# Performance work log

Hardware: AMD Instinct MI355X
Metric: run time of the kernel (lower is better)

## Reference

```python
import jax, jax.numpy as jnp
import numpy as np

D = 1024
N_HEAD = 16
EXP = 4
EPS = 1e-6


def setup_inputs() -> dict:
    key = jax.random.key(0)
    ks = jax.random.split(key, 7)
    s = 0.02
    return {
        "x": jax.random.normal(ks[0], (2, 2048, D), dtype=jnp.float32),
        "w_qkv": jax.random.normal(ks[1], (3 * D, D), dtype=jnp.float32) * s,
        "w_o": jax.random.normal(ks[2], (D, D), dtype=jnp.float32) * s,
        "w_up": jax.random.normal(ks[3], (EXP * D, D), dtype=jnp.float32) * s,
        "w_gate": jax.random.normal(ks[4], (EXP * D, D), dtype=jnp.float32) * s,
        "w_down": jax.random.normal(ks[5], (D, EXP * D), dtype=jnp.float32) * s,
        "scale1": jnp.ones((D,), dtype=jnp.float32),
        "scale2": jnp.ones((D,), dtype=jnp.float32),
    }


def rmsnorm(x, scale):
    return x / jnp.sqrt(jnp.mean(x * x, axis=-1, keepdims=True) + EPS) * scale


def attention(x, w_qkv, w_o):
    b, s, d = x.shape
    dh = d // N_HEAD
    qkv = x @ w_qkv.T  # [b,s,3d]
    q, k, v = jnp.split(qkv, 3, axis=-1)
    # [b,h,s,dh]
    q = q.reshape(b, s, N_HEAD, dh).transpose(0, 2, 1, 3)
    k = k.reshape(b, s, N_HEAD, dh).transpose(0, 2, 1, 3)
    v = v.reshape(b, s, N_HEAD, dh).transpose(0, 2, 1, 3)
    scores = jnp.einsum("bhqd,bhkd->bhqk", q, k) / jnp.sqrt(jnp.float32(dh))
    causal = jnp.tril(jnp.ones((s, s), dtype=bool))
    scores = jnp.where(causal, scores, -jnp.inf)
    attn = jax.nn.softmax(scores, axis=-1)
    out = jnp.einsum("bhqk,bhkd->bhqd", attn, v)
    out = out.transpose(0, 2, 1, 3).reshape(b, s, d)
    return out @ w_o.T


def mlp(x, w_up, w_gate, w_down):
    return (x @ w_up.T * jax.nn.silu(x @ w_gate.T)) @ w_down.T


def reference(x, w_qkv, w_o, w_up, w_gate, w_down, scale1, scale2):
    x = x + attention(rmsnorm(x, scale1), w_qkv, w_o)
    return x + mlp(rmsnorm(x, scale2), w_up, w_gate, w_down)
```

## Files before the change

kernel.cpp:

```cpp
#include <hip/hip_runtime.h>


typedef __attribute__((ext_vector_type(8))) short short8;
typedef __attribute__((ext_vector_type(4))) float floatx4;

#define EPI_NONE 0
#define EPI_RES  1
#define EPI_GATE 2
#define EPI_QKV  3

#define QSCALE 0.1803368801f

__device__ __forceinline__ float b2f(unsigned short u) {
  union { unsigned int i; float f; } c; c.i = ((unsigned int)u) << 16; return c.f;
}
__device__ __forceinline__ unsigned short f2b(float f) {
  union { float f; unsigned int u; } c; c.f = f;
  unsigned int r = 0x7fffu + ((c.u >> 16) & 1u);
  return (unsigned short)((c.u + r) >> 16);
}
__device__ __forceinline__ unsigned int f2b2(float a, float b) {
  return (unsigned int)f2b(a) | ((unsigned int)f2b(b) << 16);
}

__device__ __forceinline__ void load_lds16(const void* g, void* l) {
  __builtin_amdgcn_global_load_lds(
      (const __attribute__((address_space(1))) unsigned int*)g,
      (__attribute__((address_space(3))) unsigned int*)l, 16, 0, 0);
}

__global__ __launch_bounds__(256)
void cvt_all_kernel(const float* __restrict__ wq, const float* __restrict__ wo,
                    const float* __restrict__ wu, const float* __restrict__ wg,
                    const float* __restrict__ wd,
                    unsigned short* __restrict__ oq, unsigned short* __restrict__ oo,
                    unsigned short* __restrict__ ou, unsigned short* __restrict__ og,
                    unsigned short* __restrict__ od) {
  int i = blockIdx.x * 256 + threadIdx.x;
  const float* src; unsigned short* dst; int k;
  if (i < 786432)        { src = wq; dst = oq; k = i; }
  else if (i < 1048576)  { src = wo; dst = oo; k = i - 786432; }
  else if (i < 2097152)  { src = wu; dst = ou; k = i - 1048576; }
  else if (i < 3145728)  { src = wg; dst = og; k = i - 2097152; }
  else                   { src = wd; dst = od; k = i - 3145728; }
  float4 v = ((const float4*)src)[k];
  ushort4 o;
  o.x = f2b(v.x); o.y = f2b(v.y); o.z = f2b(v.z); o.w = f2b(v.w);
  ((ushort4*)dst)[k] = o;
}

__global__ __launch_bounds__(256)
void rmsnorm_kernel(const float* __restrict__ x,
                    const float* __restrict__ scale,
                    unsigned short* __restrict__ y) {
  const int row = blockIdx.x;
  const int tid = threadIdx.x;
  const int base = row * 1024 + tid * 4;
  float4 v = *(const float4*)(x + base);
  float ss = v.x*v.x + v.y*v.y + v.z*v.z + v.w*v.w;
#pragma unroll
  for (int d = 32; d > 0; d >>= 1) ss += __shfl_down(ss, d);
  __shared__ float red[4];
  const int wave = tid >> 6, lane = tid & 63;
  if (lane == 0) red[wave] = ss;
  __syncthreads();
  float tot = red[0] + red[1] + red[2] + red[3];
  float rs = rsqrtf(tot * (1.0f/1024.0f) + 1e-6f);
  float4 sv = *(const float4*)(scale + tid * 4);
  ushort4 o;
  o.x = f2b(v.x * rs * sv.x);
  o.y = f2b(v.y * rs * sv.y);
  o.z = f2b(v.z * rs * sv.z);
  o.w = f2b(v.w * rs * sv.w);
  *(ushort4*)(y + base) = o;
}

__global__ __launch_bounds__(256)
void rmsnorm_res2_kernel(const float* __restrict__ x,
                         const float* __restrict__ p0,
                         const float* __restrict__ p1,
                         const float* __restrict__ scale,
                         float* __restrict__ x1,
                         unsigned short* __restrict__ y) {
  const int row = blockIdx.x;
  const int tid = threadIdx.x;
  const int base = row * 1024 + tid * 4;
  float4 a = *(const float4*)(x + base);
  float4 b = *(const float4*)(p0 + base);
  float4 c = *(const float4*)(p1 + base);
  float4 v;
  v.x = a.x + b.x + c.x; v.y = a.y + b.y + c.y;
  v.z = a.z + b.z + c.z; v.w = a.w + b.w + c.w;
  *(float4*)(x1 + base) = v;
  float ss = v.x*v.x + v.y*v.y + v.z*v.z + v.w*v.w;
#pragma unroll
  for (int d = 32; d > 0; d >>= 1) ss += __shfl_down(ss, d);
  __shared__ float red[4];
  const int wave = tid >> 6, lane = tid & 63;
  if (lane == 0) red[wave] = ss;
  __syncthreads();
  float tot = red[0] + red[1] + red[2] + red[3];
  float rs = rsqrtf(tot * (1.0f/1024.0f) + 1e-6f);
  float4 sv = *(const float4*)(scale + tid * 4);
  ushort4 o;
  o.x = f2b(v.x * rs * sv.x);
  o.y = f2b(v.y * rs * sv.y);
  o.z = f2b(v.z * rs * sv.z);
  o.w = f2b(v.w * rs * sv.w);
  *(ushort4*)(y + base) = o;
}

__global__ __launch_bounds__(256)
void reduce_out_kernel(const float* __restrict__ x1,
                       const float* __restrict__ p1,
                       float* outp) {
  int i = blockIdx.x * 256 + threadIdx.x;
  float4 a = ((const float4*)x1)[i];
  float4 b = ((const float4*)p1)[i];
  float4 c = ((float4*)outp)[i];
  float4 v;
  v.x = a.x + b.x + c.x; v.y = a.y + b.y + c.y;
  v.z = a.z + b.z + c.z; v.w = a.w + b.w + c.w;
  ((float4*)outp)[i] = v;
}

template<int EPI, typename OutT, typename ResT>
__global__ __launch_bounds__(256)
void gemm_bt(const unsigned short* __restrict__ A,
             const unsigned short* __restrict__ B,
             OutT* C, const ResT* R, unsigned short* VT,
             int M, int N, int K, int ldc) {
  __shared__ __align__(16) unsigned short As[128 * 32];
  __shared__ __align__(16) unsigned short Bs[128 * 32];
  const int tid = threadIdx.x;
  const int wave = tid >> 6;
  const int lane = tid & 63;
  const int m0 = blockIdx.y * 128;
  const int n0 = blockIdx.x * 128;
  const int wm = (wave & 1) * 64;
  const int wn = (wave >> 1) * 64;
  const int frow = lane & 15;
  const int fk = (lane >> 4) * 8;

  floatx4 acc[4][4];
#pragma unroll
  for (int i = 0; i < 4; ++i)
#pragma unroll
    for (int j = 0; j < 4; ++j) acc[i][j] = (floatx4){0.f, 0.f, 0.f, 0.f};

  const int srow = lane >> 2;
  const int scol = (lane & 3) * 8;
  const unsigned short* Ag  = A + (size_t)(m0 + wave * 16 + srow) * K + scol;
  const unsigned short* Ag2 = A + (size_t)(m0 + (wave + 4) * 16 + srow) * K + scol;
  const unsigned short* Bg  = B + (size_t)(n0 + wave * 16 + srow) * K + scol;
  const unsigned short* Bg2 = B + (size_t)(n0 + (wave + 4) * 16 + srow) * K + scol;

  for (int k0 = 0; k0 < K; k0 += 32) {
    __syncthreads();
    load_lds16(Ag + k0,  &As[wave * 512]);
    load_lds16(Ag2 + k0, &As[(wave + 4) * 512]);
    load_lds16(Bg + k0,  &Bs[wave * 512]);
    load_lds16(Bg2 + k0, &Bs[(wave + 4) * 512]);
    __syncthreads();
    short8 af[4], bf[4];
#pragma unroll
    for (int i = 0; i < 4; ++i) af[i] = *(const short8*)&As[(wm + 16*i + frow)*32 + fk];
#pragma unroll
    for (int j = 0; j < 4; ++j) bf[j] = *(const short8*)&Bs[(wn + 16*j + frow)*32 + fk];
#pragma unroll
    for (int i = 0; i < 4; ++i)
#pragma unroll
      for (int j = 0; j < 4; ++j)
        acc[i][j] = __builtin_amdgcn_mfma_f32_16x16x32_bf16(af[i], bf[j], acc[i][j], 0, 0, 0);
  }

  const int g4 = (lane >> 4) * 4;

  if constexpr (EPI == EPI_QKV) {
    if (n0 >= 2048) {
#pragma unroll
      for (int i = 0; i < 4; ++i) {
        const int row0 = m0 + wm + 16*i + g4;
        const int b = row0 >> 11, s0 = row0 & 2047;
#pragma unroll
        for (int j = 0; j < 4; ++j) {
          const int col = n0 + wn + 16*j + frow;
          const int dg = col - 2048;
          const int rowv = (b << 10) + dg;
          ushort4 ov;
          ov.x = f2b(acc[i][j][0]);
          ov.y = f2b(acc[i][j][1]);
          ov.z = f2b(acc[i][j][2]);
          ov.w = f2b(acc[i][j][3]);
          *(ushort4*)(VT + (size_t)rowv * 2048 + s0) = ov;
        }
      }
      return;
    }
  }

  const float qs = (EPI == EPI_QKV && n0 < 1024) ? QSCALE : 1.0f;
#pragma unroll
  for (int i = 0; i < 4; ++i) {
#pragma unroll
    for (int r = 0; r < 4; ++r) {
      const int row = m0 + wm + 16*i + g4 + r;
#pragma unroll
      for (int j = 0; j < 4; ++j) {
        const int col = n0 + wn + 16*j + frow;
        const size_t idx = (size_t)row * ldc + col;
        float v = acc[i][j][r];
        if constexpr (EPI == EPI_RES) {
          v += (float)R[idx];
        } else if constexpr (EPI == EPI_GATE) {
          float up = b2f((unsigned short)R[idx]);
          v = up * (v / (1.f + __expf(-v)));
        } else if constexpr (EPI == EPI_QKV) {
          v *= qs;
        }
        if constexpr (sizeof(OutT) == 4) C[idx] = v;
        else                             C[idx] = f2b(v);
      }
    }
  }
}

__global__ __launch_bounds__(256)
void gemm_bt_splitk(const unsigned short* __restrict__ A,
                    const unsigned short* __restrict__ B,
                    float* __restrict__ P0, float* __restrict__ P1,
                    int M, int N, int K, int Ks) {
  __shared__ __align__(16) unsigned short As[128 * 32];
  __shared__ __align__(16) unsigned short Bs[128 * 32];
  const int tid = threadIdx.x;
  const int wave = tid >> 6;
  const int lane = tid & 63;
  const int m0 = blockIdx.y * 128;
  const int n0 = blockIdx.x * 128;
  const int z = blockIdx.z;
  float* C = z ? P1 : P0;
  const int kbase = z * Ks;
  const int wm = (wave & 1) * 64;
  const int wn = (wave >> 1) * 64;
  const int frow = lane & 15;
  const int fk = (lane >> 4) * 8;

  floatx4 acc[4][4];
#pragma unroll
  for (int i = 0; i < 4; ++i)
#pragma unroll
    for (int j = 0; j < 4; ++j) acc[i][j] = (floatx4){0.f, 0.f, 0.f, 0.f};

  const int srow = lane >> 2;
  const int scol = (lane & 3) * 8;
  const unsigned short* Ag  = A + (size_t)(m0 + wave * 16 + srow) * K + kbase + scol;
  const unsigned short* Ag2 = A + (size_t)(m0 + (wave + 4) * 16 + srow) * K + kbase + scol;
  const unsigned short* Bg  = B + (size_t)(n0 + wave * 16 + srow) * K + kbase + scol;
  const unsigned short* Bg2 = B + (size_t)(n0 + (wave + 4) * 16 + srow) * K + kbase + scol;

  for (int k0 = 0; k0 < Ks; k0 += 32) {
    __syncthreads();
    load_lds16(Ag + k0,  &As[wave * 512]);
    load_lds16(Ag2 + k0, &As[(wave + 4) * 512]);
    load_lds16(Bg + k0,  &Bs[wave * 512]);
    load_lds16(Bg2 + k0, &Bs[(wave + 4) * 512]);
    __syncthreads();
    short8 af[4], bf[4];
#pragma unroll
    for (int i = 0; i < 4; ++i) af[i] = *(const short8*)&As[(wm + 16*i + frow)*32 + fk];
#pragma unroll
    for (int j = 0; j < 4; ++j) bf[j] = *(const short8*)&Bs[(wn + 16*j + frow)*32 + fk];
#pragma unroll
    for (int i = 0; i < 4; ++i)
#pragma unroll
      for (int j = 0; j < 4; ++j)
        acc[i][j] = __builtin_amdgcn_mfma_f32_16x16x32_bf16(af[i], bf[j], acc[i][j], 0, 0, 0);
  }

  const int g4 = (lane >> 4) * 4;
#pragma unroll
  for (int i = 0; i < 4; ++i)
#pragma unroll
    for (int r = 0; r < 4; ++r) {
      const int row = m0 + wm + 16*i + g4 + r;
#pragma unroll
      for (int j = 0; j < 4; ++j) {
        const int col = n0 + wn + 16*j + frow;
        C[(size_t)row * N + col] = acc[i][j][r];
      }
    }
}

__global__ __launch_bounds__(256, 2)
void gemm_upgate(const unsigned short* __restrict__ A,
                 const unsigned short* __restrict__ Bu,
                 const unsigned short* __restrict__ Bg,
                 unsigned short* __restrict__ C, int M, int N, int K) {
  __shared__ __align__(16) unsigned short As[128 * 32];
  __shared__ __align__(16) unsigned short Bus[128 * 32];
  __shared__ __align__(16) unsigned short Bgs[128 * 32];
  const int tid = threadIdx.x;
  const int wave = tid >> 6;
  const int lane = tid & 63;
  const int m0 = blockIdx.y * 128;
  const int n0 = blockIdx.x * 128;
  const int wm = (wave & 1) * 64;
  const int wn = (wave >> 1) * 64;
  const int frow = lane & 15;
  const int fk = (lane >> 4) * 8;

  floatx4 au[4][4], ag[4][4];
#pragma unroll
  for (int i = 0; i < 4; ++i)
#pragma unroll
    for (int j = 0; j < 4; ++j) {
      au[i][j] = (floatx4){0.f, 0.f, 0.f, 0.f};
      ag[i][j] = (floatx4){0.f, 0.f, 0.f, 0.f};
    }

  const int srow = lane >> 2;
  const int scol = (lane & 3) * 8;
  const unsigned short* Ag1 = A  + (size_t)(m0 + wave * 16 + srow) * K + scol;
  const unsigned short* Ag2 = A  + (size_t)(m0 + (wave + 4) * 16 + srow) * K + scol;
  const unsigned short* Bu1 = Bu + (size_t)(n0 + wave * 16 + srow) * K + scol;
  const unsigned short* Bu2 = Bu + (size_t)(n0 + (wave + 4) * 16 + srow) * K + scol;
  const unsigned short* Bg1 = Bg + (size_t)(n0 + wave * 16 + srow) * K + scol;
  const unsigned short* Bg2 = Bg + (size_t)(n0 + (wave + 4) * 16 + srow) * K + scol;

  for (int k0 = 0; k0 < K; k0 += 32) {
    __syncthreads();
    load_lds16(Ag1 + k0, &As[wave * 512]);
    load_lds16(Ag2 + k0, &As[(wave + 4) * 512]);
    load_lds16(Bu1 + k0, &Bus[wave * 512]);
    load_lds16(Bu2 + k0, &Bus[(wave + 4) * 512]);
    load_lds16(Bg1 + k0, &Bgs[wave * 512]);
    load_lds16(Bg2 + k0, &Bgs[(wave + 4) * 512]);
    __syncthreads();
    short8 af[4], bu[4], bg[4];
#pragma unroll
    for (int i = 0; i < 4; ++i) af[i] = *(const short8*)&As[(wm + 16*i + frow)*32 + fk];
#pragma unroll
    for (int j = 0; j < 4; ++j) {
      bu[j] = *(const short8*)&Bus[(wn + 16*j + frow)*32 + fk];
      bg[j] = *(const short8*)&Bgs[(wn + 16*j + frow)*32 + fk];
    }
#pragma unroll
    for (int i = 0; i < 4; ++i)
#pragma unroll
      for (int j = 0; j < 4; ++j) {
        au[i][j] = __builtin_amdgcn_mfma_f32_16x16x32_bf16(af[i], bu[j], au[i][j], 0, 0, 0);
        ag[i][j] = __builtin_amdgcn_mfma_f32_16x16x32_bf16(af[i], bg[j], ag[i][j], 0, 0, 0);
      }
  }

  const int g4 = (lane >> 4) * 4;
#pragma unroll
  for (int i = 0; i < 4; ++i) {
#pragma unroll
    for (int r = 0; r < 4; ++r) {
      const int row = m0 + wm + 16*i + g4 + r;
#pragma unroll
      for (int j = 0; j < 4; ++j) {
        const int col = n0 + wn + 16*j + frow;
        float g = ag[i][j][r];
        float v = au[i][j][r] * (g / (1.f + __expf(-g)));
        C[(size_t)row * N + col] = f2b(v);
      }
    }
  }
}

__global__ __launch_bounds__(256, 2)
void attn_kernel(const unsigned short* __restrict__ qkv,
                 const unsigned short* __restrict__ vt,
                 unsigned short* __restrict__ out) {
  const int lin = blockIdx.x;
  const int bh = lin & 31;
  const int q_idx = lin >> 5;
  const int qblk = (q_idx < 8) ? (2 * q_idx) : (31 - 2 * q_idx);
  const int b = bh >> 4, h = bh & 15;
  const int tid = threadIdx.x, w = tid >> 6, lane = tid & 63;
  const int f = lane & 15, g = lane >> 4;
  const int fk = g * 8, g4 = g * 4;

  __shared__ __align__(16) unsigned short Ks[2][128 * 32];
  __shared__ __align__(16) unsigned short Vs[4][64 * 32];
  __shared__ __align__(16) unsigned int   pl[4][64 * 36];

  const unsigned short* Qb = qkv + (size_t)(b * 2048) * 2048 + h * 64;
  const unsigned short* Kb = Qb + 1024;
  const unsigned short* Vt = vt + ((size_t)(b * 16 + h) * 64) * 2048;

  const int q0 = qblk * 128 + w * 32;
  short8 qf[2][2];
#pragma unroll
  for (int i = 0; i < 2; ++i)
#pragma unroll
    for (int kq = 0; kq < 2; ++kq)
      qf[i][kq] = *(const short8*)(Qb + (size_t)(q0 + 16*i + f) * 2048 + kq * 32 + fk);

  float m_s[2] = {-1e30f, -1e30f}, l_s[2] = {0.f, 0.f};
  floatx4 o[4][2];
#pragma unroll
  for (int mt = 0; mt < 4; ++mt)
#pragma unroll
    for (int i = 0; i < 2; ++i) o[mt][i] = (floatx4){0.f, 0.f, 0.f, 0.f};

  const int srow = lane >> 2;
  const int scol = (lane & 3) * 8;
  unsigned int* plw = pl[w];

  for (int kb = 0; kb <= qblk; ++kb) {
    __syncthreads();
#pragma unroll
    for (int u = 0; u < 2; ++u) {
      const int seg = w + 4 * u;
#pragma unroll
      for (int kq = 0; kq < 2; ++kq)
        load_lds16(Kb + (size_t)(kb * 128 + seg * 16 + srow) * 2048 + kq * 32 + scol,
                   &Ks[kq][seg * 512]);
    }
#pragma unroll
    for (int c = 0; c < 4; ++c)
      load_lds16(Vt + (size_t)(w * 16 + srow) * 2048 + kb * 128 + c * 32 + scol,
                 &Vs[c][w * 512]);
    __syncthreads();

    const bool diag = (kb == qblk);
    const int jhi0 = diag ? 2 * w : 7;
    const int jhi1 = diag ? 2 * w + 1 : 7;

    floatx4 s[8][2];
#pragma unroll
    for (int j = 0; j < 8; ++j) {
      if (j > jhi1) continue;
      short8 kf0 = *(const short8*)&Ks[0][(16*j + f) * 32 + fk];
      short8 kf1 = *(const short8*)&Ks[1][(16*j + f) * 32 + fk];
#pragma unroll
      for (int i = 0; i < 2; ++i) {
        if (j > (i ? jhi1 : jhi0)) continue;
        s[j][i] = (floatx4){0.f, 0.f, 0.f, 0.f};
        s[j][i] = __builtin_amdgcn_mfma_f32_16x16x32_bf16(kf0, qf[i][0], s[j][i], 0, 0, 0);
        s[j][i] = __builtin_amdgcn_mfma_f32_16x16x32_bf16(kf1, qf[i][1], s[j][i], 0, 0, 0);
      }
    }
    if (diag) {
#pragma unroll
      for (int i = 0; i < 2; ++i) {
        const int qo = 32 * w + 16 * i + f;
        const int jh = i ? jhi1 : jhi0;
#pragma unroll
        for (int j = 0; j < 8; ++j) {
          if (j > jh) continue;
#pragma unroll
          for (int r = 0; r < 4; ++r)
            if (16 * j + g4 + r > qo) s[j][i][r] = -1e30f;
        }
      }
    }
#pragma unroll
    for (int i = 0; i < 2; ++i) {
      const int jh = i ? jhi1 : jhi0;
      float mx = -1e30f;
#pragma unroll
      for (int j = 0; j < 8; ++j) {
        if (j > jh) continue;
#pragma unroll
        for (int r = 0; r < 4; ++r) mx = fmaxf(mx, s[j][i][r]);
      }
      mx = fmaxf(mx, __shfl_xor(mx, 16));
      mx = fmaxf(mx, __shfl_xor(mx, 32));
      const float mnew = fmaxf(m_s[i], mx);
      const float alpha = exp2f(m_s[i] - mnew);
      float rs = 0.f;
#pragma unroll
      for (int j = 0; j < 8; ++j) {
        if (j > jh) continue;
#pragma unroll
        for (int r = 0; r < 4; ++r) {
          float pv = exp2f(s[j][i][r] - mnew);
          s[j][i][r] = pv;
          rs += pv;
        }
      }
      rs += __shfl_xor(rs, 16);
      rs += __shfl_xor(rs, 32);
      l_s[i] = l_s[i] * alpha + rs;
      m_s[i] = mnew;
#pragma unroll
      for (int mt = 0; mt < 4; ++mt) o[mt][i] *= alpha;
    }
#pragma unroll
    for (int i = 0; i < 2; ++i) {
      const int jh = i ? jhi1 : jhi0;
#pragma unroll
      for (int j = 0; j < 8; ++j) {
        if (j > jh) continue;
        plw[(8*j + 2*g + 0) * 36 + 16*i + f] = f2b2(s[j][i][0], s[j][i][1]);
        plw[(8*j + 2*g + 1) * 36 + 16*i + f] = f2b2(s[j][i][2], s[j][i][3]);
      }
    }
    if (diag) {
      plw[(8*(2*w + 1) + 2*g + 0) * 36 + f] = 0u;
      plw[(8*(2*w + 1) + 2*g + 1) * 36 + f] = 0u;
    }
    const int chi = diag ? w : 3;
#pragma unroll
    for (int c = 0; c < 4; ++c) {
      if (c > chi) continue;
      union { unsigned int d[4]; short8 v; } pb[2];
#pragma unroll
      for (int i = 0; i < 2; ++i)
#pragma unroll
        for (int k = 0; k < 4; ++k)
          pb[i].d[k] = plw[(16*c + 4*g + k) * 36 + 16*i + f];
#pragma unroll
      for (int mt = 0; mt < 4; ++mt) {
        short8 va = *(const short8*)&Vs[c][(16*mt + f) * 32 + fk];
#pragma unroll
        for (int i = 0; i < 2; ++i)
          o[mt][i] = __builtin_amdgcn_mfma_f32_16x16x32_bf16(va, pb[i].v, o[mt][i], 0, 0, 0);
      }
    }
  }

#pragma unroll
  for (int i = 0; i < 2; ++i) {
    const float inv = 1.0f / l_s[i];
    unsigned short* orow = out + (size_t)(b * 2048 + q0 + 16*i + f) * 1024 + h * 64;
#pragma unroll
    for (int mt = 0; mt < 4; ++mt) {
      ushort4 ov;
      ov.x = f2b(o[mt][i][0] * inv);
      ov.y = f2b(o[mt][i][1] * inv);
      ov.z = f2b(o[mt][i][2] * inv);
      ov.w = f2b(o[mt][i][3] * inv);
      *(ushort4*)(orow + 16 * mt + g4) = ov;
    }
  }
}

extern "C" void kernel_launch(void* const* d_in, const int* in_sizes, int n_in,
                              void* d_out, int out_size, void* d_ws, size_t ws_size,
                              hipStream_t stream) {
  const float* x      = (const float*)d_in[0];
  const float* w_qkv  = (const float*)d_in[1];
  const float* w_o    = (const float*)d_in[2];
  const float* w_up   = (const float*)d_in[3];
  const float* w_gate = (const float*)d_in[4];
  const float* w_down = (const float*)d_in[5];
  const float* scale1 = (const float*)d_in[6];
  const float* scale2 = (const float*)d_in[7];

  char* ws = (char*)d_ws;
  unsigned short* wq_b = (unsigned short*)(ws);
  unsigned short* wo_b = (unsigned short*)(ws +  6291456);
  unsigned short* wu_b = (unsigned short*)(ws +  8388608);
  unsigned short* wg_b = (unsigned short*)(ws + 16777216);
  unsigned short* wd_b = (unsigned short*)(ws + 25165824);
  unsigned short* qkv  = (unsigned short*)(ws + 33554432);
  unsigned short* hup  = (unsigned short*)(ws + 33554432);
  unsigned short* vT   = (unsigned short*)(ws + 50331648);
  unsigned short* attnb= (unsigned short*)(ws + 58720256);
  unsigned short* xn   = (unsigned short*)(ws + 67108864);
  float*          x1   = (float*)         (ws + 75497472);
  float*          outp = (float*)d_out;

  float* wo_p0   = (float*)(ws + 33554432);
  float* wo_p1   = (float*)d_out;
  float* down_p0 = (float*)d_out;
  float* down_p1 = (float*)(ws + 8388608);

  const int M = 4096;
  dim3 blk(256);

  cvt_all_kernel<<<16384, blk, 0, stream>>>(w_qkv, w_o, w_up, w_gate, w_down,
                                            wq_b, wo_b, wu_b, wg_b, wd_b);

  rmsnorm_kernel<<<4096, blk, 0, stream>>>(x, scale1, xn);
  gemm_bt<EPI_QKV, unsigned short, unsigned short>
      <<<dim3(24, 32), blk, 0, stream>>>(xn, wq_b, qkv, (const unsigned short*)nullptr, vT,
                                         M, 3072, 1024, 2048);
  attn_kernel<<<dim3(512), blk, 0, stream>>>(qkv, vT, attnb);
  gemm_bt_splitk<<<dim3(8, 32, 2), blk, 0, stream>>>(attnb, wo_b, wo_p0, wo_p1,
                                                     M, 1024, 1024, 512);

  rmsnorm_res2_kernel<<<4096, blk, 0, stream>>>(x, wo_p0, wo_p1, scale2, x1, xn);

  gemm_upgate<<<dim3(32, 32), blk, 0, stream>>>(xn, wu_b, wg_b, hup, M, 4096, 1024);
  gemm_bt_splitk<<<dim3(8, 32, 2), blk, 0, stream>>>(hup, wd_b, down_p0, down_p1,
                                                     M, 1024, 4096, 2048);
  reduce_out_kernel<<<4096, blk, 0, stream>>>(x1, down_p1, outp);

  (void)in_sizes; (void)n_in; (void)out_size; (void)ws_size;
}
```

Baseline: 414.6 us.

## Replace up/gate GEMM with 256x128 double-buffered pipelined 512-thread kernel

Rewrites the fused up/gate projection GEMM to use 256x128 output tiles with 8 waves, 64-wide K steps, and a two-stage LDS buffer (128 KB dynamic shared memory). Global-to-LDS loads for the next K tile are interleaved with MFMA quarters, using explicit barriers, waitcnts and setprio. It also adds XOR swizzling of LDS to avoid bank conflicts and a block-index swizzle for L2 locality. The aim is to hide memory latency and raise MFMA utilisation in the largest GEMM. In exchange the kernel hardcodes K=1024 and N=4096, and needs a large LDS allocation that limits occupancy.

```diff
diff --git a/kernel.cpp b/kernel.cpp
--- a/kernel.cpp
+++ b/kernel.cpp
@@ -291,80 +291,163 @@
     }
 }
 
-__global__ __launch_bounds__(256, 2)
-void gemm_upgate(const unsigned short* __restrict__ A,
-                 const unsigned short* __restrict__ Bu,
-                 const unsigned short* __restrict__ Bg,
-                 unsigned short* __restrict__ C, int M, int N, int K) {
-  __shared__ __align__(16) unsigned short As[128 * 32];
-  __shared__ __align__(16) unsigned short Bus[128 * 32];
-  __shared__ __align__(16) unsigned short Bgs[128 * 32];
-  const int tid = threadIdx.x;
+
+#define A_OFF(q,h) (((q)*2+(h))*8192)
+#define B_OFF(q,h) (32768 + ((q)*2+(h))*8192)
+
+#define GBAR() __builtin_amdgcn_s_barrier()
+#define WLG()  asm volatile("s_waitcnt lgkmcnt(0)" ::: "memory")
+#define WVM(N) asm volatile("s_waitcnt vmcnt(" #N ")" ::: "memory")
+
+#define STAGE(LB, SRC, T) do {                                               \
+    const unsigned short* _s = (SRC) + (size_t)r0 * 1024 + (T) * 64 + gs;    \
+    load_lds16(_s,             &lds[(LB) + wave * 512]);                     \
+    load_lds16(_s + 64 * 1024, &lds[(LB) + 4096 + wave * 512]);              \
+  } while (0)
+
+#define LDA4(dst, q, h) do {                                                 \
+    const unsigned short* _b = &lds[A_OFF(q,h) + arow];                      \
+    _Pragma("unroll")                                                        \
+    for (int _i = 0; _i < 4; ++_i) {                                         \
+      dst[_i][0] = *(const short8*)(_b + _i * 1024 + g0);                    \
+      dst[_i][1] = *(const short8*)(_b + _i * 1024 + g1);                    \
+    }                                                                        \
+  } while (0)
+
+#define LDB2(dst, q, h) do {                                                 \
+    const unsigned short* _b = &lds[B_OFF(q,h) + brow];                      \
+    _Pragma("unroll")                                                        \
+    for (int _j = 0; _j < 2; ++_j) {                                         \
+      dst[_j][0] = *(const short8*)(_b + _j * 1024 + g0);                    \
+      dst[_j][1] = *(const short8*)(_b + _j * 1024 + g1);                    \
+    }                                                                        \
+  } while (0)
+
+#define MMQ(aa, bb, IO, JO) do {                                             \
+    _Pragma("unroll")                                                        \
+    for (int _i = 0; _i < 4; ++_i)                                           \
+      _Pragma("unroll")                                                      \
+      for (int _j = 0; _j < 2; ++_j) {                                       \
+        acc[(IO)+_i][(JO)+_j] = __builtin_amdgcn_mfma_f32_16x16x32_bf16(     \
+            aa[_i][0], bb[_j][0], acc[(IO)+_i][(JO)+_j], 0, 0, 0);           \
+        acc[(IO)+_i][(JO)+_j] = __builtin_amdgcn_mfma_f32_16x16x32_bf16(     \
+            aa[_i][1], bb[_j][1], acc[(IO)+_i][(JO)+_j], 0, 0, 0);           \
+      }                                                                      \
+  } while (0)
+
+__global__ __launch_bounds__(512, 2)
+void gemm256_upgate(const unsigned short* __restrict__ A,
+                    const unsigned short* __restrict__ Bu,
+                    const unsigned short* __restrict__ Bg,
+                    unsigned short* __restrict__ C) {
+  extern __shared__ __align__(16) unsigned short lds[];
+  const int tid  = threadIdx.x;
   const int wave = tid >> 6;
   const int lane = tid & 63;
-  const int m0 = blockIdx.y * 128;
-  const int n0 = blockIdx.x * 128;
-  const int wm = (wave & 1) * 64;
-  const int wn = (wave >> 1) * 64;
+  const int wr   = wave >> 2;
+  const int wc   = wave & 3;
   const int frow = lane & 15;
-  const int fk = (lane >> 4) * 8;
-
-  floatx4 au[4][4], ag[4][4];
-#pragma unroll
-  for (int i = 0; i < 4; ++i)
-#pragma unroll
-    for (int j = 0; j < 4; ++j) {
-      au[i][j] = (floatx4){0.f, 0.f, 0.f, 0.f};
-      ag[i][j] = (floatx4){0.f, 0.f, 0.f, 0.f};
-    }
-
-  const int srow = lane >> 2;
-  const int scol = (lane & 3) * 8;
-  const unsigned short* Ag1 = A  + (size_t)(m0 + wave * 16 + srow) * K + scol;
-  const unsigned short* Ag2 = A  + (size_t)(m0 + (wave + 4) * 16 + srow) * K + scol;
-  const unsigned short* Bu1 = Bu + (size_t)(n0 + wave * 16 + srow) * K + scol;
-  const unsigned short* Bu2 = Bu + (size_t)(n0 + (wave + 4) * 16 + srow) * K + scol;
-  const unsigned short* Bg1 = Bg + (size_t)(n0 + wave * 16 + srow) * K + scol;
-  const unsigned short* Bg2 = Bg + (size_t)(n0 + (wave + 4) * 16 + srow) * K + scol;
-
-  for (int k0 = 0; k0 < K; k0 += 32) {
-    __syncthreads();
-    load_lds16(Ag1 + k0, &As[wave * 512]);
-    load_lds16(Ag2 + k0, &As[(wave + 4) * 512]);
-    load_lds16(Bu1 + k0, &Bus[wave * 512]);
-    load_lds16(Bu2 + k0, &Bus[(wave + 4) * 512]);
-    load_lds16(Bg1 + k0, &Bgs[wave * 512]);
-    load_lds16(Bg2 + k0, &Bgs[(wave + 4) * 512]);
-    __syncthreads();
-    short8 af[4], bu[4], bg[4];
-#pragma unroll
-    for (int i = 0; i < 4; ++i) af[i] = *(const short8*)&As[(wm + 16*i + frow)*32 + fk];
-#pragma unroll
-    for (int j = 0; j < 4; ++j) {
-      bu[j] = *(const short8*)&Bus[(wn + 16*j + frow)*32 + fk];
-      bg[j] = *(const short8*)&Bgs[(wn + 16*j + frow)*32 + fk];
-    }
-#pragma unroll
-    for (int i = 0; i < 4; ++i)
-#pragma unroll
-      for (int j = 0; j < 4; ++j) {
-        au[i][j] = __builtin_amdgcn_mfma_f32_16x16x32_bf16(af[i], bu[j], au[i][j], 0, 0, 0);
-        ag[i][j] = __builtin_amdgcn_mfma_f32_16x16x32_bf16(af[i], bg[j], ag[i][j], 0, 0, 0);
-      }
-  }
-
-  const int g4 = (lane >> 4) * 4;
-#pragma unroll
-  for (int i = 0; i < 4; ++i) {
-#pragma unroll
-    for (int r = 0; r < 4; ++r) {
-      const int row = m0 + wm + 16*i + g4 + r;
-#pragma unroll
-      for (int j = 0; j < 4; ++j) {
-        const int col = n0 + wn + 16*j + frow;
-        float g = ag[i][j][r];
-        float v = au[i][j][r] * (g / (1.f + __expf(-g)));
-        C[(size_t)row * N + col] = f2b(v);
+  const int s4   = lane >> 4;
+
+  const int orig = blockIdx.x;
+  const int swz  = (orig & 7) * 64 + (orig >> 3);
+  const int bx   = swz & 31;
+  const int by   = swz >> 5;
+  const int m0   = by * 256;
+  const int n0   = bx * 128;
+
+  const int f7 = frow & 7;
+  const int g0 = ((0 + s4) ^ f7) * 8;
+  const int g1 = ((4 + s4) ^ f7) * 8;
+  const int arow = (wr * 64 + frow) * 64;
+  const int brow = (wc * 32 + frow) * 64;
+
+  const int r0 = wave * 8 + (lane >> 3);
+  const int gs = ((lane & 7) ^ (lane >> 3)) * 8;
+
+  const unsigned short* Asrc  = A  + (size_t)m0 * 1024;
+  const unsigned short* B0src = Bu + (size_t)(bx * 128) * 1024;
+  const unsigned short* B1src = Bg + (size_t)(bx * 128) * 1024;
+
+  floatx4 acc[8][4];
+#pragma unroll
+  for (int i = 0; i < 8; ++i)
+#pragma unroll
+    for (int j = 0; j < 4; ++j) acc[i][j] = (floatx4){0.f, 0.f, 0.f, 0.f};
+
+  STAGE(A_OFF(0,0), Asrc, 0);
+  STAGE(B_OFF(0,0), B0src, 0);
+  STAGE(B_OFF(0,1), B1src, 0);
+  STAGE(A_OFF(0,1), Asrc + 128 * 1024, 0);
+  WVM(4);
+  STAGE(A_OFF(1,0), Asrc, 1);
+  STAGE(B_OFF(1,0), B0src, 1);
+  STAGE(B_OFF(1,1), B1src, 1);
+  WVM(6);
+  GBAR();
+
+  short8 af0[4][2], af1[4][2], bf0[2][2], bf1[2][2];
+
+  for (int it = 0; it < 8; ++it) {
+    const int t   = it * 2;
+    const int tn2 = (t + 2) & 15;
+    const int tn3 = (t + 3) & 15;
+    LDA4(af0, 0, 0);
+    LDB2(bf0, 0, 0);
+    STAGE(A_OFF(1,1), Asrc + 128 * 1024, (t + 1) & 15);
+    GBAR(); WLG();
+    __builtin_amdgcn_s_setprio(1); MMQ(af0, bf0, 0, 0); __builtin_amdgcn_s_setprio(0);
+    GBAR();
+    LDB2(bf1, 0, 1);
+    STAGE(A_OFF(0,0), Asrc, tn2);
+    GBAR(); WLG();
+    __builtin_amdgcn_s_setprio(1); MMQ(af0, bf1, 0, 2); __builtin_amdgcn_s_setprio(0);
+    GBAR();
+    LDA4(af1, 0, 1);
+    STAGE(B_OFF(0,0), B0src, tn2);
+    GBAR(); WLG();
+    __builtin_amdgcn_s_setprio(1); MMQ(af1, bf0, 4, 0); __builtin_amdgcn_s_setprio(0);
+    GBAR();
+    STAGE(B_OFF(0,1), B1src, tn2);
+    GBAR();
+    __builtin_amdgcn_s_setprio(1); MMQ(af1, bf1, 4, 2); __builtin_amdgcn_s_setprio(0);
+    WVM(6);
+    GBAR();
+    LDA4(af0, 1, 0);
+    LDB2(bf0, 1, 0);
+    STAGE(A_OFF(0,1), Asrc + 128 * 1024, tn2);
+    GBAR(); WLG();
+    __builtin_amdgcn_s_setprio(1); MMQ(af0, bf0, 0, 0); __builtin_amdgcn_s_setprio(0);
+    GBAR();
+    LDB2(bf1, 1, 1);
+    STAGE(A_OFF(1,0), Asrc, tn3);
+    GBAR(); WLG();
+    __builtin_amdgcn_s_setprio(1); MMQ(af0, bf1, 0, 2); __builtin_amdgcn_s_setprio(0);
+    GBAR();
+    LDA4(af1, 1, 1);
+    STAGE(B_OFF(1,0), B0src, tn3);
+    GBAR(); WLG();
+    __builtin_amdgcn_s_setprio(1); MMQ(af1, bf0, 4, 0); __builtin_amdgcn_s_setprio(0);
+    GBAR();
+    STAGE(B_OFF(1,1), B1src, tn3);
+    GBAR();
+    __builtin_amdgcn_s_setprio(1); MMQ(af1, bf1, 4, 2); __builtin_amdgcn_s_setprio(0);
+    WVM(6);
+    GBAR();
+  }
+  asm volatile("s_waitcnt vmcnt(0)" ::: "memory");
+
+#pragma unroll
+  for (int i = 0; i < 8; ++i) {
+    const int row = m0 + (i >> 2) * 128 + wr * 64 + (i & 3) * 16 + s4 * 4;
+#pragma unroll
+    for (int j = 0; j < 2; ++j) {
+      const int col = n0 + wc * 32 + j * 16 + frow;
+#pragma unroll
+      for (int r = 0; r < 4; ++r) {
+        const float g = acc[i][j + 2][r];
+        const float v = acc[i][j][r] * (g / (1.f + __expf(-g)));
+        C[(size_t)(row + r) * 4096 + col] = f2b(v);
       }
     }
   }
@@ -574,6 +657,13 @@
   const int M = 4096;
   dim3 blk(256);
 
+  static int lds_opted = 0;
+  if (!lds_opted) {
+    hipFuncSetAttribute((const void*)gemm256_upgate,
+                        hipFuncAttributeMaxDynamicSharedMemorySize, 131072);
+    lds_opted = 1;
+  }
+
   cvt_all_kernel<<<16384, blk, 0, stream>>>(w_qkv, w_o, w_up, w_gate, w_down,
                                             wq_b, wo_b, wu_b, wg_b, wd_b);
 
@@ -587,7 +677,7 @@
 
   rmsnorm_res2_kernel<<<4096, blk, 0, stream>>>(x, wo_p0, wo_p1, scale2, x1, xn);
 
-  gemm_upgate<<<dim3(32, 32), blk, 0, stream>>>(xn, wu_b, wg_b, hup, M, 4096, 1024);
+  gemm256_upgate<<<dim3(512), dim3(512), 131072, stream>>>(xn, wu_b, wg_b, hup);
   gemm_bt_splitk<<<dim3(8, 32, 2), blk, 0, stream>>>(hup, wd_b, down_p0, down_p1,
                                                      M, 1024, 4096, 2048);
   reduce_out_kernel<<<4096, blk, 0, stream>>>(x1, down_p1, outp);
```

New measurement: 416.9 us. Within noise of the previous version (+0.5%).
